# Performance work log

Measured on AMD Instinct MI355X. Metric: run time of the kernel, lower is better.

Reference implementation:

```python
import jax, jax.numpy as jnp
import numpy as np

B, LP, LH, D, H = 32, 1024, 1024, 256, 256

def setup_inputs() -> dict:
    key = jax.random.key(0)
    k1, k2, k3 = jax.random.split(key, 3)
    premises = jax.random.normal(k1, (B, LP, D), dtype=jnp.float32)
    hypotheses = jax.random.normal(k2, (B, LH, D), dtype=jnp.float32)
    W_F = jax.random.normal(k3, (D, H), dtype=jnp.float32) * (1.0 / np.sqrt(D))
    return {"premises": premises, "hypotheses": hypotheses, "W_F": W_F}

def reference(premises, hypotheses, W_F):
    # Tanh-projected features: F_p = tanh(P @ W_F), F_h = tanh(H @ W_F)
    F_p = jnp.tanh(jnp.einsum('bpd,dh->bph', premises, W_F))   # [B,LP,H]
    F_h = jnp.tanh(jnp.einsum('bqd,dh->bqh', hypotheses, W_F)) # [B,LH,H]
    # Alignment scores e_ij = F_p . F_h
    eijs = jnp.einsum('bph,bqh->bpq', F_p, F_h)                # [B,LP,LH]
    # betas: for each premise token, softmax over hypothesis tokens, weighted sum of hypotheses
    betas = jnp.einsum('bpq,bqd->bpd', jax.nn.softmax(eijs, axis=-1), hypotheses)  # [B,LP,D]
    # alphas: for each hypothesis token, softmax over premise tokens, weighted sum of premises
    alphas = jnp.einsum('bqp,bpd->bqd',
                        jax.nn.softmax(jnp.swapaxes(eijs, 1, 2), axis=-1),
                        premises)                                                   # [B,LH,D]
    return betas, alphas
```

## Files before the change

### kernel.cpp

```cpp
#include <hip/hip_runtime.h>

typedef _Float16 f16;
typedef __attribute__((ext_vector_type(4))) _Float16 f16x4;
typedef __attribute__((ext_vector_type(8))) _Float16 f16x8;
typedef __attribute__((ext_vector_type(4))) float f32x4;
typedef __attribute__((ext_vector_type(16))) float f32x16;
typedef unsigned int u32;

#define BB 32
#define LL 1024
#define DD 256

#define VMCNT(N) asm volatile("s_waitcnt vmcnt(" #N ")" ::: "memory")
#define LGKMCNT0 asm volatile("s_waitcnt lgkmcnt(0)" ::: "memory")

__device__ __forceinline__ void async_copy16(const f16* g, f16* l) {
  __builtin_amdgcn_global_load_lds(
      (const __attribute__((address_space(1))) u32*)(const void*)g,
      (__attribute__((address_space(3))) u32*)(void*)l, 16, 0, 0);
}

__device__ __forceinline__ u32 pack_pkrtz(float a, float b) {
  auto pk = __builtin_amdgcn_cvt_pkrtz(a, b);
  u32 w;
  __builtin_memcpy(&w, &pk, 4);
  return w;
}


__global__ __launch_bounds__(256) void w_to_frag(const float* __restrict__ W,
                                                 f16* __restrict__ WtF) {
  __shared__ float T32[256][33];
  const int tid = threadIdx.x;
  const int N = blockIdx.x;
  const int nn = tid & 31, kr = tid >> 5;
#pragma unroll
  for (int p = 0; p < 32; ++p) {
    int k = p * 8 + kr;
    T32[k][nn] = W[(size_t)k * 256 + N * 32 + nn];
  }
  __syncthreads();
  const int wv = tid >> 6, lane = tid & 63;
  const int l32 = lane & 31, half = lane >> 5;
#pragma unroll
  for (int i = 0; i < 4; ++i) {
    int s = wv * 4 + i;
    f16x8 ov;
#pragma unroll
    for (int j = 0; j < 8; ++j) ov[j] = (f16)T32[s * 16 + half * 8 + j][l32];
    *(f16x8*)&WtF[(size_t)N * 8192 + s * 512 + lane * 8] = ov;
  }
}

__global__ __launch_bounds__(256, 3) void proj_mfma(
    const float* __restrict__ Pin, const float* __restrict__ Hin,
    const f16* __restrict__ WtF, f16* __restrict__ Fp, f16* __restrict__ Fh,
    f16* __restrict__ Vtp, f16* __restrict__ Vth) {
  __shared__ f16 As[64][264];
  const int tid = threadIdx.x;
  const int wv = tid >> 6, lane = tid & 63;
  const int l32 = lane & 31, half = lane >> 5;
  const int wm = wv >> 1, wn = wv & 1;
  const float* A = blockIdx.z ? Hin : Pin;
  f16* F = blockIdx.z ? Fh : Fp;
  f16* VtO = blockIdx.z ? Vth : Vtp;
  const int m0 = blockIdx.x * 64;
  const int T0 = m0 >> 5;

  {
    const int r = tid >> 4;
    const int c4 = (tid & 15) * 4;
#pragma unroll
    for (int pp = 0; pp < 4; ++pp)
#pragma unroll
      for (int ch = 0; ch < 4; ++ch) {
        float4 v =
            *(const float4*)&A[(size_t)(m0 + r + pp * 16) * 256 + ch * 64 + c4];
        f16x4 h4;
        h4[0] = (f16)v.x; h4[1] = (f16)v.y; h4[2] = (f16)v.z; h4[3] = (f16)v.w;
        *(f16x4*)&As[r + pp * 16][ch * 64 + c4] = h4;
      }
  }
  __syncthreads();

  f16x8 af[16];
#pragma unroll
  for (int ks = 0; ks < 16; ++ks)
    af[ks] = *(const f16x8*)&As[wm * 32 + l32][ks * 16 + half * 8];

  {
#pragma unroll
    for (int i = 0; i < 8; ++i) {
      int idx = wv * 8 + i;
      int Tl = idx >> 4;
      int t = (idx >> 1) & 7;
      int qh = idx & 1;
      int qb = Tl * 32 + qh * 16 + half * 8;
      f16x8 ov;
#pragma unroll
      for (int j = 0; j < 8; ++j) ov[j] = As[qb + j][t * 32 + l32];
      *(f16x8*)&VtO[(size_t)(T0 + Tl) * 8192 + t * 1024 + qh * 512 +
                    half * 256 + l32 * 8] = ov;
    }
  }
  __syncthreads();

#pragma unroll
  for (int nc = 0; nc < 4; ++nc) {
    f32x16 acc = (f32x16)(0.f);
#pragma unroll
    for (int ks = 0; ks < 16; ++ks) {
      f16x8 wf = *(const f16x8*)&WtF[(size_t)nc * 16384 + wn * 8192 +
                                     ks * 512 + lane * 8];
      acc = __builtin_amdgcn_mfma_f32_32x32x16_f16(af[ks], wf, acc, 0, 0, 0);
    }
#pragma unroll
    for (int r = 0; r < 16; ++r) {
      float xv = acc[r];
      float e2 = __expf(2.f * xv);
      float th = 1.f - 2.f / (e2 + 1.f);
      As[wm * 32 + (r & 3) + 8 * (r >> 2) + 4 * half]
        [nc * 64 + wn * 32 + l32] = (f16)th;
    }
  }
  __syncthreads();

#pragma unroll
  for (int i = 0; i < 8; ++i) {
    int idx = wv * 8 + i;
    int Tl = idx >> 4;
    int s = idx & 15;
    f16x8 ov = *(const f16x8*)&As[Tl * 32 + l32][s * 16 + half * 8];
    *(f16x8*)&F[(size_t)(T0 + Tl) * 8192 + s * 512 + half * 256 + l32 * 8] =
        ov;
  }
}

__global__ __launch_bounds__(512, 2) void flash_mfma(
    const f16* __restrict__ Fpm, const f16* __restrict__ Fhm,
    const f16* __restrict__ Vth, const f16* __restrict__ Vtp,
    float* __restrict__ Out) {
  __shared__ f16 SMEM[4][8192];

  const int tid = threadIdx.x;
  const int wv = tid >> 6, lane = tid & 63;
  const int l32 = lane & 31, half = lane >> 5;

  const f16* Fq = Fpm;
  const f16* Fk = Fhm;
  const f16* Vt = Vth;
  float* O = Out;
  if (blockIdx.y) { Fq = Fhm; Fk = Fpm; Vt = Vtp; O = Out + (size_t)BB * LL * DD; }

  const int x = blockIdx.x;
  const int b = ((x >> 5) << 3) | (x & 7);
  const int pblk = (x >> 3) & 3;
  const int p0 = pblk * 256 + wv * 32;
  const int p = p0 + l32;

  const f16* Fq_b = Fq + (size_t)b * LL * DD;
  const f16* Fk_b = Fk + (size_t)b * LL * DD;
  const f16* Vt_b = Vt + (size_t)b * LL * DD;

  f16x8 qf[16];
  {
    const f16* qt = Fq_b + (size_t)(p >> 5) * 8192 + half * 256 + (p & 31) * 8;
#pragma unroll
    for (int s = 0; s < 16; ++s) qf[s] = *(const f16x8*)&qt[s * 512];
  }

  float m_run = -1e30f, l_run = 0.f;
  f32x16 o[8];
#pragma unroll
  for (int t = 0; t < 8; ++t) o[t] = (f32x16)(0.f);

  auto stage_K = [&](int buf, int T) {
    const f16* kt = Fk_b + (size_t)T * 8192 + wv * 1024 + lane * 8;
    async_copy16(kt, &SMEM[buf][wv * 1024]);
    async_copy16(kt + 512, &SMEM[buf][wv * 1024 + 512]);
  };
  auto stage_V = [&](int buf, int T) {
    const f16* vt = Vt_b + (size_t)T * 8192 + wv * 1024 + lane * 8;
    async_copy16(vt, &SMEM[2 + buf][wv * 1024]);
    async_copy16(vt + 512, &SMEM[2 + buf][wv * 1024 + 512]);
  };

  auto qk16 = [&](int buf) {
    f32x16 S = (f32x16)(0.f);
    __builtin_amdgcn_s_setprio(1);
#pragma unroll
    for (int s = 0; s < 16; ++s) {
      f16x8 kf = *(const f16x8*)&SMEM[buf][s * 512 + lane * 8];
      S = __builtin_amdgcn_mfma_f32_32x32x16_f16(kf, qf[s], S, 0, 0, 0);
    }
    __builtin_amdgcn_s_setprio(0);
    return S;
  };

  f16x8 pf[2];
  auto softmax_pack = [&](const f32x16& S) {
    float mt = S[0];
#pragma unroll
    for (int r = 1; r < 16; ++r) mt = fmaxf(mt, S[r]);
    mt = fmaxf(mt, __shfl_xor(mt, 32, 64));
    const bool keep = __all((int)(mt - m_run <= 8.0f)) != 0;
    const float mn = keep ? m_run : fmaxf(m_run, mt);
    float pe[16];
    float ts = 0.f;
#pragma unroll
    for (int r = 0; r < 16; ++r) {
      pe[r] = __expf(S[r] - mn);
      ts += pe[r];
    }
    ts += __shfl_xor(ts, 32, 64);
    if (!keep) {
      const float alpha = __expf(m_run - mn);
      l_run *= alpha;
      m_run = mn;
#pragma unroll
      for (int t = 0; t < 8; ++t)
#pragma unroll
        for (int r = 0; r < 16; ++r) o[t][r] *= alpha;
    }
    l_run += ts;

    u32 pw[8];
#pragma unroll
    for (int i = 0; i < 8; ++i) pw[i] = pack_pkrtz(pe[2 * i], pe[2 * i + 1]);
    u32 rc[4];
    {
      u32 s0 = half ? pw[0] : pw[2];
      u32 s1 = half ? pw[1] : pw[3];
      u32 s2 = half ? pw[4] : pw[6];
      u32 s3 = half ? pw[5] : pw[7];
      rc[0] = (u32)__shfl_xor((int)s0, 32, 64);
      rc[1] = (u32)__shfl_xor((int)s1, 32, 64);
      rc[2] = (u32)__shfl_xor((int)s2, 32, 64);
      rc[3] = (u32)__shfl_xor((int)s3, 32, 64);
    }
#pragma unroll
    for (int h = 0; h < 2; ++h) {
      u32 tmp[4];
      tmp[0] = half ? rc[2 * h] : pw[4 * h];
      tmp[1] = half ? rc[2 * h + 1] : pw[4 * h + 1];
      tmp[2] = half ? pw[4 * h + 2] : rc[2 * h];
      tmp[3] = half ? pw[4 * h + 3] : rc[2 * h + 1];
      __builtin_memcpy(&pf[h], tmp, 16);
    }
  };

  auto pv = [&](int buf) {
    __builtin_amdgcn_s_setprio(1);
#pragma unroll
    for (int t = 0; t < 8; ++t) {
      f16x8 v0 = *(const f16x8*)&SMEM[2 + buf][t * 1024 + lane * 8];
      o[t] = __builtin_amdgcn_mfma_f32_32x32x16_f16(v0, pf[0], o[t], 0, 0, 0);
      f16x8 v1 = *(const f16x8*)&SMEM[2 + buf][t * 1024 + 512 + lane * 8];
      o[t] = __builtin_amdgcn_mfma_f32_32x32x16_f16(v1, pf[1], o[t], 0, 0, 0);
    }
    __builtin_amdgcn_s_setprio(0);
  };

  stage_K(0, 0);
  stage_V(0, 0);
  stage_K(1, 1);
  VMCNT(2);
  __builtin_amdgcn_sched_barrier(0);
  __builtin_amdgcn_s_barrier();
  f32x16 Scur = qk16(0);
  stage_V(1, 1);

  for (int it = 0; it < 31; ++it) {
    const int cur = it & 1, nxt = cur ^ 1;
    if (it < 30) {
      stage_K(cur, it + 2);
      VMCNT(2);
    } else {
      VMCNT(0);
    }
    __builtin_amdgcn_sched_barrier(0);
    __builtin_amdgcn_s_barrier();
    f32x16 Snext = qk16(nxt);
    softmax_pack(Scur);
    pv(cur);
    __builtin_amdgcn_s_barrier();
    if (it < 30) stage_V(cur, it + 2);
    Scur = Snext;
  }
  softmax_pack(Scur);
  pv(1);
  __syncthreads();

  const float inv = 1.f / l_run;
  float* Tw = (float*)&SMEM[0][0] + wv * (32 * 36);
  float* Ob = O + (size_t)b * LL * DD;
#pragma unroll
  for (int t = 0; t < 8; ++t) {
#pragma unroll
    for (int g = 0; g < 4; ++g) {
      int C = 2 * g + half;
      f32x4 v;
      v[0] = o[t][4 * g + 0] * inv;
      v[1] = o[t][4 * g + 1] * inv;
      v[2] = o[t][4 * g + 2] * inv;
      v[3] = o[t][4 * g + 3] * inv;
      *(f32x4*)&Tw[l32 * 36 + C * 4] = v;
    }
    LGKMCNT0;
#pragma unroll
    for (int pass = 0; pass < 4; ++pass) {
      int row = pass * 8 + (lane >> 3);
      int Cr = lane & 7;
      f32x4 v = *(const f32x4*)&Tw[row * 36 + Cr * 4];
      *(f32x4*)&Ob[(size_t)(p0 + row) * DD + t * 32 + Cr * 4] = v;
    }
    LGKMCNT0;
  }
}

extern "C" void kernel_launch(void* const* d_in, const int* in_sizes, int n_in,
                              void* d_out, int out_size, void* d_ws,
                              size_t ws_size, hipStream_t stream) {
  const float* premises = (const float*)d_in[0];
  const float* hypotheses = (const float*)d_in[1];
  const float* W = (const float*)d_in[2];
  float* out = (float*)d_out;

  const size_t MF = (size_t)BB * LL * DD;
  f16* Fp = (f16*)d_ws;
  f16* Fh = Fp + MF;
  f16* Vth = Fh + MF;
  f16* Vtp = Vth + MF;
  f16* WtF = (f16*)((char*)d_out + (size_t)out_size * 4 - 256 * 256 * 2);

  w_to_frag<<<dim3(8), 256, 0, stream>>>(W, WtF);
  proj_mfma<<<dim3(512, 1, 2), 256, 0, stream>>>(premises, hypotheses, WtF, Fp,
                                                 Fh, Vtp, Vth);
  flash_mfma<<<dim3(128, 2), 512, 0, stream>>>(Fp, Fh, Vth, Vtp, out);
}
```

Before: 205.4 us.

## Triple-buffer V tiles and issue K/V prefetches together before compute

Adds a third shared-memory buffer for the V tiles. The V prefetch for tile it+2 is now issued together with the K prefetch at the top of each iteration, instead of after the trailing barrier once PV is done. This gives V loads more time in flight and removes the global-load issue from the tail of the loop. The cost is shared memory growing from 64KB to 80KB per block, which may limit occupancy at two blocks per CU. The vmcnt wait is also stricter than needed, since it waits for V(it+1) as well.

```diff
diff --git a/kernel.cpp b/kernel.cpp
--- a/kernel.cpp
+++ b/kernel.cpp
@@ -140,7 +140,7 @@
     const f16* __restrict__ Fpm, const f16* __restrict__ Fhm,
     const f16* __restrict__ Vth, const f16* __restrict__ Vtp,
     float* __restrict__ Out) {
-  __shared__ f16 SMEM[4][8192];
+  __shared__ f16 SMEM[5][8192];
 
   const int tid = threadIdx.x;
   const int wv = tid >> 6, lane = tid & 63;
@@ -174,23 +174,23 @@
 #pragma unroll
   for (int t = 0; t < 8; ++t) o[t] = (f32x16)(0.f);
 
-  auto stage_K = [&](int buf, int T) {
+  auto stage_K = [&](int slot, int T) {
     const f16* kt = Fk_b + (size_t)T * 8192 + wv * 1024 + lane * 8;
-    async_copy16(kt, &SMEM[buf][wv * 1024]);
-    async_copy16(kt + 512, &SMEM[buf][wv * 1024 + 512]);
-  };
-  auto stage_V = [&](int buf, int T) {
+    async_copy16(kt, &SMEM[slot][wv * 1024]);
+    async_copy16(kt + 512, &SMEM[slot][wv * 1024 + 512]);
+  };
+  auto stage_V = [&](int slot, int T) {
     const f16* vt = Vt_b + (size_t)T * 8192 + wv * 1024 + lane * 8;
-    async_copy16(vt, &SMEM[2 + buf][wv * 1024]);
-    async_copy16(vt + 512, &SMEM[2 + buf][wv * 1024 + 512]);
-  };
-
-  auto qk16 = [&](int buf) {
+    async_copy16(vt, &SMEM[2 + slot][wv * 1024]);
+    async_copy16(vt + 512, &SMEM[2 + slot][wv * 1024 + 512]);
+  };
+
+  auto qk16 = [&](int slot) {
     f32x16 S = (f32x16)(0.f);
     __builtin_amdgcn_s_setprio(1);
 #pragma unroll
     for (int s = 0; s < 16; ++s) {
-      f16x8 kf = *(const f16x8*)&SMEM[buf][s * 512 + lane * 8];
+      f16x8 kf = *(const f16x8*)&SMEM[slot][s * 512 + lane * 8];
       S = __builtin_amdgcn_mfma_f32_32x32x16_f16(kf, qf[s], S, 0, 0, 0);
     }
     __builtin_amdgcn_s_setprio(0);
@@ -249,13 +249,13 @@
     }
   };
 
-  auto pv = [&](int buf) {
+  auto pv = [&](int slot) {
     __builtin_amdgcn_s_setprio(1);
 #pragma unroll
     for (int t = 0; t < 8; ++t) {
-      f16x8 v0 = *(const f16x8*)&SMEM[2 + buf][t * 1024 + lane * 8];
+      f16x8 v0 = *(const f16x8*)&SMEM[2 + slot][t * 1024 + lane * 8];
       o[t] = __builtin_amdgcn_mfma_f32_32x32x16_f16(v0, pf[0], o[t], 0, 0, 0);
-      f16x8 v1 = *(const f16x8*)&SMEM[2 + buf][t * 1024 + 512 + lane * 8];
+      f16x8 v1 = *(const f16x8*)&SMEM[2 + slot][t * 1024 + 512 + lane * 8];
       o[t] = __builtin_amdgcn_mfma_f32_32x32x16_f16(v1, pf[1], o[t], 0, 0, 0);
     }
     __builtin_amdgcn_s_setprio(0);
@@ -264,31 +264,30 @@
   stage_K(0, 0);
   stage_V(0, 0);
   stage_K(1, 1);
-  VMCNT(2);
+  stage_V(1, 1);
+  VMCNT(4);
   __builtin_amdgcn_sched_barrier(0);
   __builtin_amdgcn_s_barrier();
   f32x16 Scur = qk16(0);
-  stage_V(1, 1);
 
   for (int it = 0; it < 31; ++it) {
-    const int cur = it & 1, nxt = cur ^ 1;
     if (it < 30) {
-      stage_K(cur, it + 2);
-      VMCNT(2);
+      stage_K(it & 1, it + 2);
+      stage_V((it + 2) % 3, it + 2);
+      VMCNT(4);
     } else {
       VMCNT(0);
     }
     __builtin_amdgcn_sched_barrier(0);
     __builtin_amdgcn_s_barrier();
-    f32x16 Snext = qk16(nxt);
+    f32x16 Snext = qk16((it + 1) & 1);
     softmax_pack(Scur);
-    pv(cur);
+    pv(it % 3);
     __builtin_amdgcn_s_barrier();
-    if (it < 30) stage_V(cur, it + 2);
     Scur = Snext;
   }
   softmax_pack(Scur);
-  pv(1);
+  pv(31 % 3);
   __syncthreads();
 
   const float inv = 1.f / l_run;
```

Result: slower. 209.6 us (+2.0%).
